# Performance work log

Hardware: AMD Instinct MI355X
Metric: run time of the kernel (lower is better)

Reference implementation:

```python
import jax, jax.numpy as jnp
import numpy as np

B, S, D = 4, 2048, 1024
H = 16
HD = D // H  # 64


def _xavier(key, shape):
    fan_in, fan_out = shape[1], shape[0]
    limit = float(np.sqrt(6.0 / (fan_in + fan_out)))
    return jax.random.uniform(key, shape, jnp.float32, -limit, limit)


def setup_inputs() -> dict:
    key = jax.random.key(0)
    ks = jax.random.split(key, 5)
    x = jax.random.normal(ks[0], (B, S, D), dtype=jnp.float32)
    # nn.Linear weights are [out, in]; biases zero-initialized
    Wq = _xavier(ks[1], (D, D)); bq = jnp.zeros((D,), jnp.float32)
    Wk = _xavier(ks[2], (D, D)); bk = jnp.zeros((D,), jnp.float32)
    Wv = _xavier(ks[3], (D, D)); bv = jnp.zeros((D,), jnp.float32)
    Wo = _xavier(ks[4], (D, D)); bo = jnp.zeros((D,), jnp.float32)
    return {"x": x, "Wq": Wq, "bq": bq, "Wk": Wk, "bk": bk,
            "Wv": Wv, "bv": bv, "Wo": Wo, "bo": bo}


def reference(x, Wq, bq, Wk, bk, Wv, bv, Wo, bo):
    # Projections (torch Linear: y = x @ W.T + b), reshape to [B, H, S, HD]
    def proj(W, b):
        y = jnp.einsum('bsd,ed->bse', x, W) + b
        return y.reshape(B, S, H, HD).transpose(0, 2, 1, 3)

    q = proj(Wq, bq)
    k = proj(Wk, bk)
    v = proj(Wv, bv)

    scale = 1.0 / jnp.sqrt(jnp.float32(HD))
    scores = jnp.einsum('bhqd,bhkd->bhqk', q, k) * scale  # [B,H,S,S]
    probs = jax.nn.softmax(scores, axis=-1)
    ctx = jnp.einsum('bhqk,bhkd->bhqd', probs, v)  # [B,H,S,HD]
    ctx = ctx.transpose(0, 2, 1, 3).reshape(B, S, D)
    out = jnp.einsum('bsd,ed->bse', ctx, Wo) + bo
    return out
```

## Files before the change

### kernel.cpp

```cpp
#include <hip/hip_runtime.h>
#include <hip/hip_bf16.h>
#include <stdint.h>


typedef __bf16 bf16;
typedef __bf16 bf16x8 __attribute__((ext_vector_type(8)));
typedef __bf16 bf16x4 __attribute__((ext_vector_type(4)));
typedef float  f32x4  __attribute__((ext_vector_type(4)));

#define MFMA_BF16(A, B, C) __builtin_amdgcn_mfma_f32_16x16x32_bf16(A, B, C, 0, 0, 0)
#define EXP2F(x) __builtin_amdgcn_exp2f(x)

#define ASYNC_CP16(DST_LDS, SRC_G)                                            \
  __builtin_amdgcn_global_load_lds(                                           \
      (__attribute__((address_space(1))) void*)(SRC_G),                       \
      (__attribute__((address_space(3))) void*)(DST_LDS), 16, 0, 0)

__global__ __launch_bounds__(256) void cvt5(
    const float* __restrict__ s0, bf16* __restrict__ d0, int n0,
    const float* __restrict__ s1, bf16* __restrict__ d1, int n1,
    const float* __restrict__ s2, bf16* __restrict__ d2, int n2,
    const float* __restrict__ s3, bf16* __restrict__ d3, int n3,
    const float* __restrict__ s4, bf16* __restrict__ d4, int n4)
{
  const float* s; bf16* d; int n;
  switch (blockIdx.y) {
    case 0: s = s0; d = d0; n = n0; break;
    case 1: s = s1; d = d1; n = n1; break;
    case 2: s = s2; d = d2; n = n2; break;
    case 3: s = s3; d = d3; n = n3; break;
    default: s = s4; d = d4; n = n4; break;
  }
  const int stride = gridDim.x * blockDim.x * 4;
  for (int i = (blockIdx.x * blockDim.x + threadIdx.x) * 4; i < n; i += stride) {
    const float4 v = *(const float4*)(s + i);
    bf16x4 o;
    o[0] = (bf16)v.x; o[1] = (bf16)v.y; o[2] = (bf16)v.z; o[3] = (bf16)v.w;
    *(bf16x4*)(d + i) = o;
  }
}

__global__ __launch_bounds__(256, 4) void gemm_qkv(
    const bf16* __restrict__ X,
    const bf16* __restrict__ Wq, const bf16* __restrict__ Wk,
    const bf16* __restrict__ Wv,
    const float* __restrict__ bq, const float* __restrict__ bk,
    const float* __restrict__ bv,
    bf16* __restrict__ Qo, bf16* __restrict__ Ko, bf16* __restrict__ Vo,
    float qscale)
{
  constexpr int N = 1024, K = 1024;
  __shared__ alignas(16) bf16 As[8192];
  __shared__ alignas(16) bf16 Bs[8192];

  const int sel = blockIdx.x >> 3;
  const bf16*  W    = (sel == 0) ? Wq : (sel == 1) ? Wk : Wv;
  const float* bias = (sel == 0) ? bq : (sel == 1) ? bk : bv;
  bf16*        Y    = (sel == 0) ? Qo : (sel == 1) ? Ko : Vo;
  const float scale = (sel == 0) ? qscale : 1.0f;

  const int tid  = threadIdx.x;
  const int lane = tid & 63;
  const int wv   = tid >> 6;
  const int l15  = lane & 15;
  const int quad = lane >> 4;
  const int wm   = (wv >> 1) * 64;
  const int wn   = (wv & 1) * 64;
  const int nbase = (blockIdx.x & 7) * 128;
  const int mbase = blockIdx.y * 128;

  f32x4 acc[4][4];
  #pragma unroll
  for (int i = 0; i < 4; ++i)
    #pragma unroll
    for (int j = 0; j < 4; ++j)
      acc[i][j] = (f32x4){0.f, 0.f, 0.f, 0.f};

  const int r8 = lane >> 3;
  const int oc = (lane & 7) ^ r8;
  const size_t lrowA = (size_t)(mbase + wv * 32 + r8);
  const size_t lrowB = (size_t)(nbase + wv * 32 + r8);

  for (int kb = 0; kb < K; kb += 64) {
    #pragma unroll
    for (int c = 0; c < 4; ++c) {
      ASYNC_CP16(As + (wv * 32 + c * 8) * 64, X + (lrowA + c * 8) * K + kb + oc * 8);
      ASYNC_CP16(Bs + (wv * 32 + c * 8) * 64, W + (lrowB + c * 8) * K + kb + oc * 8);
    }
    __syncthreads();
    #pragma unroll
    for (int ks = 0; ks < 2; ++ks) {
      bf16x8 af[4], bfr[4];
      #pragma unroll
      for (int t = 0; t < 4; ++t) {
        const int ma = wm + t * 16 + l15;
        af[t]  = *(const bf16x8*)(As + (ma * 8 + ((ks * 4 + quad) ^ (ma & 7))) * 8);
        const int nb = wn + t * 16 + l15;
        bfr[t] = *(const bf16x8*)(Bs + (nb * 8 + ((ks * 4 + quad) ^ (nb & 7))) * 8);
      }
      #pragma unroll
      for (int i = 0; i < 4; ++i)
        #pragma unroll
        for (int j = 0; j < 4; ++j)
          acc[i][j] = MFMA_BF16(af[i], bfr[j], acc[i][j]);
    }
    __syncthreads();
  }

  #pragma unroll
  for (int i = 0; i < 4; ++i) {
    const int row0 = mbase + wm + i * 16 + quad * 4;
    #pragma unroll
    for (int j = 0; j < 4; ++j) {
      const int col = nbase + wn + j * 16 + l15;
      const float bv2 = bias[col];
      #pragma unroll
      for (int r = 0; r < 4; ++r) {
        const float v = (acc[i][j][r] + bv2) * scale;
        const int row = row0 + r;
        if (sel != 2) {
          Y[(size_t)row * N + col] = (bf16)v;
        } else {
          const int bb = row >> 11, s  = row & 2047;
          const int hh = col >> 6,  hd = col & 63;
          Y[(size_t)((bb * 16 + hh) * 64 + hd) * 2048 + s] = (bf16)v;
        }
      }
    }
  }
}

__global__ __launch_bounds__(256, 4) void gemm_o(
    const bf16* __restrict__ X, const bf16* __restrict__ W,
    const float* __restrict__ bias, float* __restrict__ Yf)
{
  constexpr int N = 1024, K = 1024;
  __shared__ alignas(16) bf16 As[8192];
  __shared__ alignas(16) bf16 Bs[4096];

  const int tid  = threadIdx.x;
  const int lane = tid & 63;
  const int wv   = tid >> 6;
  const int l15  = lane & 15;
  const int quad = lane >> 4;
  const int wm   = (wv >> 1) * 64;
  const int wn   = (wv & 1) * 32;
  const int nbase = blockIdx.x * 64;
  const int mbase = blockIdx.y * 128;

  f32x4 acc[4][2];
  #pragma unroll
  for (int i = 0; i < 4; ++i)
    #pragma unroll
    for (int j = 0; j < 2; ++j)
      acc[i][j] = (f32x4){0.f, 0.f, 0.f, 0.f};

  const int r8 = lane >> 3;
  const int oc = (lane & 7) ^ r8;
  const size_t lrowA = (size_t)(mbase + wv * 32 + r8);
  const size_t lrowB = (size_t)(nbase + wv * 16 + r8);

  for (int kb = 0; kb < K; kb += 64) {
    #pragma unroll
    for (int c = 0; c < 4; ++c)
      ASYNC_CP16(As + (wv * 32 + c * 8) * 64, X + (lrowA + c * 8) * K + kb + oc * 8);
    #pragma unroll
    for (int c = 0; c < 2; ++c)
      ASYNC_CP16(Bs + (wv * 16 + c * 8) * 64, W + (lrowB + c * 8) * K + kb + oc * 8);
    __syncthreads();
    #pragma unroll
    for (int ks = 0; ks < 2; ++ks) {
      bf16x8 af[4], bfr[2];
      #pragma unroll
      for (int t = 0; t < 4; ++t) {
        const int ma = wm + t * 16 + l15;
        af[t] = *(const bf16x8*)(As + (ma * 8 + ((ks * 4 + quad) ^ (ma & 7))) * 8);
      }
      #pragma unroll
      for (int t = 0; t < 2; ++t) {
        const int nb = wn + t * 16 + l15;
        bfr[t] = *(const bf16x8*)(Bs + (nb * 8 + ((ks * 4 + quad) ^ (nb & 7))) * 8);
      }
      #pragma unroll
      for (int i = 0; i < 4; ++i)
        #pragma unroll
        for (int j = 0; j < 2; ++j)
          acc[i][j] = MFMA_BF16(af[i], bfr[j], acc[i][j]);
    }
    __syncthreads();
  }

  #pragma unroll
  for (int i = 0; i < 4; ++i) {
    const int row0 = mbase + wm + i * 16 + quad * 4;
    #pragma unroll
    for (int j = 0; j < 2; ++j) {
      const int col = nbase + wn + j * 16 + l15;
      const float bv2 = bias[col];
      #pragma unroll
      for (int r = 0; r < 4; ++r)
        Yf[(size_t)(row0 + r) * N + col] = acc[i][j][r] + bv2;
    }
  }
}

__global__ __launch_bounds__(256, 4) void attn(
    const bf16* __restrict__ Qb, const bf16* __restrict__ Kb,
    const bf16* __restrict__ Vt, bf16* __restrict__ Ob)
{
  constexpr int S = 2048, D = 1024;
  __shared__ alignas(16) bf16 Ks[2][4096];
  __shared__ alignas(16) bf16 Vs[2][4096];

  const int tid  = threadIdx.x;
  const int lane = tid & 63;
  const int wv   = tid >> 6;
  const int l15  = lane & 15;
  const int q0   = lane >> 4;
  const int b = blockIdx.z, h = blockIdx.y;
  const int qblk = blockIdx.x * 128 + wv * 32;

  bf16x8 qf[2][2];
  #pragma unroll
  for (int qt = 0; qt < 2; ++qt)
    #pragma unroll
    for (int dh = 0; dh < 2; ++dh)
      qf[qt][dh] = *(const bf16x8*)(
          Qb + (size_t)(b * S + qblk + qt * 16 + l15) * D + h * 64 + dh * 32 + q0 * 8);

  float lrun[2] = {0.f, 0.f};
  f32x4 o[4][2];
  #pragma unroll
  for (int ht = 0; ht < 4; ++ht)
    #pragma unroll
    for (int qt = 0; qt < 2; ++qt)
      o[ht][qt] = (f32x4){0.f, 0.f, 0.f, 0.f};

  const int skey = lane;
  const int so   = wv;
  const bf16* kg = Kb + (size_t)(b * S) * D + h * 64;
  const bf16* vg = Vt + (size_t)((b * 16 + h) * 64) * S;
  const int swk = (skey & 3) | (((skey >> 3) & 1) << 2);

  const int kla = 8 * (l15 >> 2) + (l15 & 3);
  const int swa = (l15 & 3) | (((l15 >> 2) & 1) << 2);
  const int swv = l15 & 7;

#define STAGE(KC, BUF)                                                        \
  {                                                                           \
    const bf16* krow = kg + (size_t)((KC) + skey) * D;                        \
    const bf16x8 k0 = *(const bf16x8*)(krow + so * 8);                        \
    const bf16x8 k1 = *(const bf16x8*)(krow + (so + 4) * 8);                  \
    *(bf16x8*)(&Ks[BUF][(skey * 8 + (so ^ swk)) * 8]) = k0;                   \
    *(bf16x8*)(&Ks[BUF][(skey * 8 + ((so + 4) ^ swk)) * 8]) = k1;             \
    const bf16* vrow = vg + (size_t)skey * S + (KC);                          \
    const bf16x8 v0 = *(const bf16x8*)(vrow + so * 8);                        \
    const bf16x8 v1 = *(const bf16x8*)(vrow + (so + 4) * 8);                  \
    *(bf16x8*)(&Vs[BUF][(skey * 8 + (so ^ (skey & 7))) * 8]) = v0;            \
    *(bf16x8*)(&Vs[BUF][(skey * 8 + ((so + 4) ^ (skey & 7))) * 8]) = v1;      \
  }

  STAGE(0, 0);

  for (int kc = 0, it = 0; kc < S; kc += 64, ++it) {
    const int cur = it & 1;
    __syncthreads();
    if (kc + 64 < S) STAGE(kc + 64, cur ^ 1);

    f32x4 sc[2][4];
    #pragma unroll
    for (int kt = 0; kt < 4; ++kt) {
      const int key = kla + 4 * (kt & 1) + 32 * (kt >> 1);
      const bf16x8 kf0 = *(const bf16x8*)(&Ks[cur][(key * 8 + (q0 ^ swa)) * 8]);
      const bf16x8 kf1 = *(const bf16x8*)(&Ks[cur][(key * 8 + ((q0 + 4) ^ swa)) * 8]);
      #pragma unroll
      for (int qt = 0; qt < 2; ++qt) {
        f32x4 s = MFMA_BF16(kf0, qf[qt][0], ((f32x4){0.f, 0.f, 0.f, 0.f}));
        sc[qt][kt] = MFMA_BF16(kf1, qf[qt][1], s);
      }
    }

    bf16x8 pb[2][2];
    #pragma unroll
    for (int qt = 0; qt < 2; ++qt) {
      float ps = 0.f;
      #pragma unroll
      for (int kt = 0; kt < 4; ++kt)
        #pragma unroll
        for (int r = 0; r < 4; ++r) {
          const float p = EXP2F(sc[qt][kt][r]);
          ps += p;
          pb[qt][kt >> 1][(kt & 1) * 4 + r] = (bf16)p;
        }
      lrun[qt] += ps;
    }

    #pragma unroll
    for (int ht = 0; ht < 4; ++ht) {
      const int row = ht * 16 + l15;
      const bf16x8 vf0 = *(const bf16x8*)(&Vs[cur][(row * 8 + (q0 ^ swv)) * 8]);
      const bf16x8 vf1 = *(const bf16x8*)(&Vs[cur][(row * 8 + ((q0 + 4) ^ swv)) * 8]);
      #pragma unroll
      for (int qt = 0; qt < 2; ++qt) {
        o[ht][qt] = MFMA_BF16(vf0, pb[qt][0], o[ht][qt]);
        o[ht][qt] = MFMA_BF16(vf1, pb[qt][1], o[ht][qt]);
      }
    }
  }
#undef STAGE

  #pragma unroll
  for (int qt = 0; qt < 2; ++qt) {
    float l = lrun[qt];
    l += __shfl_xor(l, 16, 64);
    l += __shfl_xor(l, 32, 64);
    const float inv = 1.0f / l;
    bf16* orow = Ob + (size_t)(b * S + qblk + qt * 16 + l15) * D + h * 64 + q0 * 4;
    #pragma unroll
    for (int ht = 0; ht < 4; ++ht) {
      bf16x4 w;
      w[0] = (bf16)(o[ht][qt][0] * inv);
      w[1] = (bf16)(o[ht][qt][1] * inv);
      w[2] = (bf16)(o[ht][qt][2] * inv);
      w[3] = (bf16)(o[ht][qt][3] * inv);
      *(bf16x4*)(orow + ht * 16) = w;
    }
  }
}

extern "C" void kernel_launch(void* const* d_in, const int* in_sizes, int n_in,
                              void* d_out, int out_size, void* d_ws, size_t ws_size,
                              hipStream_t stream)
{
  const float* x  = (const float*)d_in[0];
  const float* Wq = (const float*)d_in[1];
  const float* bq = (const float*)d_in[2];
  const float* Wk = (const float*)d_in[3];
  const float* bk = (const float*)d_in[4];
  const float* Wv = (const float*)d_in[5];
  const float* bv = (const float*)d_in[6];
  const float* Wo = (const float*)d_in[7];
  const float* bo = (const float*)d_in[8];
  float* out = (float*)d_out;

  const size_t NX = (size_t)8192 * 1024;
  const size_t NW = (size_t)1024 * 1024;

  bf16* xb  = (bf16*)d_ws;
  bf16* Wqb = xb  + NX;
  bf16* Wkb = Wqb + NW;
  bf16* Wvb = Wkb + NW;
  bf16* Wob = Wvb + NW;
  bf16* Qb  = Wob + NW;
  bf16* Kb  = Qb  + NX;
  bf16* Vt  = Kb  + NX;
  bf16* Ctx = Vt  + NX;

  const float QSCALE = 0.18033688011112042f;

  dim3 bc(256, 1, 1);
  hipLaunchKernelGGL(cvt5, dim3(1024, 5, 1), bc, 0, stream,
                     x, xb, (int)NX, Wq, Wqb, (int)NW, Wk, Wkb, (int)NW,
                     Wv, Wvb, (int)NW, Wo, Wob, (int)NW);

  hipLaunchKernelGGL(gemm_qkv, dim3(24, 64, 1), bc, 0, stream,
                     xb, Wqb, Wkb, Wvb, bq, bk, bv, Qb, Kb, Vt, QSCALE);

  hipLaunchKernelGGL(attn, dim3(16, 16, 4), bc, 0, stream, Qb, Kb, Vt, Ctx);

  hipLaunchKernelGGL(gemm_o, dim3(16, 64, 1), bc, 0, stream, Ctx, Wob, bo, out);
}
```

Before: 293.3 us.

## Tile V-transpose layout for async LDS staging in attention; widen gemm_o tile

The QKV GEMM now writes V-transposed in 64-key tiles, so each tile of 64 head-dims by 64 keys is contiguous. The attention kernel can then stage K and V into shared memory with direct async global-to-LDS copies instead of register round-trips, with XOR swizzles built into the source offsets. Separately, the output projection GEMM tile is widened from 128x64 to 128x128, doubling accumulators per wave and dropping the occupancy hint in the launch bounds. The intent is to cut staging instructions and VGPR pressure in attention and to raise data reuse in gemm_o, at the cost of more registers and fewer blocks there.

```diff
diff --git a/kernel.cpp b/kernel.cpp
--- a/kernel.cpp
+++ b/kernel.cpp
@@ -123,20 +123,21 @@
         } else {
           const int bb = row >> 11, s  = row & 2047;
           const int hh = col >> 6,  hd = col & 63;
-          Y[(size_t)((bb * 16 + hh) * 64 + hd) * 2048 + s] = (bf16)v;
+          Y[(size_t)(bb * 16 + hh) * (2048 * 64) + (size_t)(s >> 6) * 4096 +
+            hd * 64 + (s & 63)] = (bf16)v;
         }
       }
     }
   }
 }
 
-__global__ __launch_bounds__(256, 4) void gemm_o(
+__global__ __launch_bounds__(256) void gemm_o(
     const bf16* __restrict__ X, const bf16* __restrict__ W,
     const float* __restrict__ bias, float* __restrict__ Yf)
 {
   constexpr int N = 1024, K = 1024;
   __shared__ alignas(16) bf16 As[8192];
-  __shared__ alignas(16) bf16 Bs[4096];
+  __shared__ alignas(16) bf16 Bs[8192];
 
   const int tid  = threadIdx.x;
   const int lane = tid & 63;
@@ -144,47 +145,43 @@
   const int l15  = lane & 15;
   const int quad = lane >> 4;
   const int wm   = (wv >> 1) * 64;
-  const int wn   = (wv & 1) * 32;
-  const int nbase = blockIdx.x * 64;
+  const int wn   = (wv & 1) * 64;
+  const int nbase = blockIdx.x * 128;
   const int mbase = blockIdx.y * 128;
 
-  f32x4 acc[4][2];
+  f32x4 acc[4][4];
   #pragma unroll
   for (int i = 0; i < 4; ++i)
     #pragma unroll
-    for (int j = 0; j < 2; ++j)
+    for (int j = 0; j < 4; ++j)
       acc[i][j] = (f32x4){0.f, 0.f, 0.f, 0.f};
 
   const int r8 = lane >> 3;
   const int oc = (lane & 7) ^ r8;
   const size_t lrowA = (size_t)(mbase + wv * 32 + r8);
-  const size_t lrowB = (size_t)(nbase + wv * 16 + r8);
+  const size_t lrowB = (size_t)(nbase + wv * 32 + r8);
 
   for (int kb = 0; kb < K; kb += 64) {
     #pragma unroll
-    for (int c = 0; c < 4; ++c)
+    for (int c = 0; c < 4; ++c) {
       ASYNC_CP16(As + (wv * 32 + c * 8) * 64, X + (lrowA + c * 8) * K + kb + oc * 8);
-    #pragma unroll
-    for (int c = 0; c < 2; ++c)
-      ASYNC_CP16(Bs + (wv * 16 + c * 8) * 64, W + (lrowB + c * 8) * K + kb + oc * 8);
+      ASYNC_CP16(Bs + (wv * 32 + c * 8) * 64, W + (lrowB + c * 8) * K + kb + oc * 8);
+    }
     __syncthreads();
     #pragma unroll
     for (int ks = 0; ks < 2; ++ks) {
-      bf16x8 af[4], bfr[2];
+      bf16x8 af[4], bfr[4];
       #pragma unroll
       for (int t = 0; t < 4; ++t) {
         const int ma = wm + t * 16 + l15;
-        af[t] = *(const bf16x8*)(As + (ma * 8 + ((ks * 4 + quad) ^ (ma & 7))) * 8);
-      }
-      #pragma unroll
-      for (int t = 0; t < 2; ++t) {
+        af[t]  = *(const bf16x8*)(As + (ma * 8 + ((ks * 4 + quad) ^ (ma & 7))) * 8);
         const int nb = wn + t * 16 + l15;
         bfr[t] = *(const bf16x8*)(Bs + (nb * 8 + ((ks * 4 + quad) ^ (nb & 7))) * 8);
       }
       #pragma unroll
       for (int i = 0; i < 4; ++i)
         #pragma unroll
-        for (int j = 0; j < 2; ++j)
+        for (int j = 0; j < 4; ++j)
           acc[i][j] = MFMA_BF16(af[i], bfr[j], acc[i][j]);
     }
     __syncthreads();
@@ -194,7 +191,7 @@
   for (int i = 0; i < 4; ++i) {
     const int row0 = mbase + wm + i * 16 + quad * 4;
     #pragma unroll
-    for (int j = 0; j < 2; ++j) {
+    for (int j = 0; j < 4; ++j) {
       const int col = nbase + wn + j * 16 + l15;
       const float bv2 = bias[col];
       #pragma unroll
@@ -236,29 +233,26 @@
     for (int qt = 0; qt < 2; ++qt)
       o[ht][qt] = (f32x4){0.f, 0.f, 0.f, 0.f};
 
-  const int skey = lane;
-  const int so   = wv;
-  const bf16* kg = Kb + (size_t)(b * S) * D + h * 64;
-  const bf16* vg = Vt + (size_t)((b * 16 + h) * 64) * S;
-  const int swk = (skey & 3) | (((skey >> 3) & 1) << 2);
+  const int r8a = lane >> 3;
+  const int oc1 = (lane & 7) ^ (r8a & 3);
+  const int oc2 = oc1 ^ 4;
+  const int ov  = (lane & 7) ^ r8a;
+  const bf16* kgw = Kb + (size_t)(b * S) * D + h * 64 + (size_t)(16 * wv) * D;
+  const bf16* vgw = Vt + (size_t)(b * 16 + h) * (2048 * 64) + (16 * wv) * 64;
+
+#define STAGE(KC, BUF)                                                        \
+  {                                                                           \
+    const bf16* ks = kgw + (size_t)(KC) * D;                                  \
+    ASYNC_CP16(&Ks[BUF][wv * 1024],       ks + (size_t)r8a * D + oc1 * 8);    \
+    ASYNC_CP16(&Ks[BUF][wv * 1024 + 512], ks + (size_t)(8 + r8a) * D + oc2 * 8);\
+    const bf16* vs = vgw + (KC) * 64;                                         \
+    ASYNC_CP16(&Vs[BUF][wv * 1024],       vs + r8a * 64 + ov * 8);            \
+    ASYNC_CP16(&Vs[BUF][wv * 1024 + 512], vs + (8 + r8a) * 64 + ov * 8);      \
+  }
 
   const int kla = 8 * (l15 >> 2) + (l15 & 3);
   const int swa = (l15 & 3) | (((l15 >> 2) & 1) << 2);
   const int swv = l15 & 7;
-
-#define STAGE(KC, BUF)                                                        \
-  {                                                                           \
-    const bf16* krow = kg + (size_t)((KC) + skey) * D;                        \
-    const bf16x8 k0 = *(const bf16x8*)(krow + so * 8);                        \
-    const bf16x8 k1 = *(const bf16x8*)(krow + (so + 4) * 8);                  \
-    *(bf16x8*)(&Ks[BUF][(skey * 8 + (so ^ swk)) * 8]) = k0;                   \
-    *(bf16x8*)(&Ks[BUF][(skey * 8 + ((so + 4) ^ swk)) * 8]) = k1;             \
-    const bf16* vrow = vg + (size_t)skey * S + (KC);                          \
-    const bf16x8 v0 = *(const bf16x8*)(vrow + so * 8);                        \
-    const bf16x8 v1 = *(const bf16x8*)(vrow + (so + 4) * 8);                  \
-    *(bf16x8*)(&Vs[BUF][(skey * 8 + (so ^ (skey & 7))) * 8]) = v0;            \
-    *(bf16x8*)(&Vs[BUF][(skey * 8 + ((so + 4) ^ (skey & 7))) * 8]) = v1;      \
-  }
 
   STAGE(0, 0);
 
@@ -368,5 +362,5 @@
 
   hipLaunchKernelGGL(attn, dim3(16, 16, 4), bc, 0, stream, Qb, Kb, Vt, Ctx);
 
-  hipLaunchKernelGGL(gemm_o, dim3(16, 64, 1), bc, 0, stream, Ctx, Wob, bo, out);
-}
+  hipLaunchKernelGGL(gemm_o, dim3(8, 64, 1), bc, 0, stream, Ctx, Wob, bo, out);
+}
```

Result: no change. 291.9 us (-0.5%).
